# Kernel optimization log

Measured on AMD Instinct MI355X. Metric: run time of the kernel, lower is better.

The kernel has to match this reference:

```python
import jax, jax.numpy as jnp
import numpy as np

K = 4
EPS = 1e-6
NEG_INF = -1e9


def _extract_patches(x, k):
    # x: [C, H, W] -> [P, C*k*k], P = (H-k+1)*(W-k+1), p = hp*Wp + wp
    C, H, W = x.shape
    Hp, Wp = H - k + 1, W - k + 1
    cols = jnp.stack([x[:, di:di + Hp, dj:dj + Wp]
                      for di in range(k) for dj in range(k)], axis=1)  # [C, k*k, Hp, Wp]
    return cols.reshape(C * k * k, Hp * Wp).T  # [P, C*k*k]


def setup_inputs() -> dict:
    key = jax.random.key(0)
    k1, k2, k3 = jax.random.split(key, 3)
    C, H, W = 32, 80, 80
    low = jax.random.normal(k1, (1, C, H, W), dtype=jnp.float32)
    high = jax.random.normal(k2, (1, C, H, W), dtype=jnp.float32)
    mask = jax.random.randint(k3, (H + 1, W + 1), 0, 2, dtype=jnp.int32)
    return {"low_level_features": low, "hight_level_features": high, "mask": mask}


def reference(low_level_features, hight_level_features, mask):
    k = K
    low = low_level_features[0]    # [C, H, W]
    high = hight_level_features[0]
    C, H, W = low.shape
    Hp, Wp = H - k + 1, W - k + 1
    P = Hp * Wp

    low_p = _extract_patches(low, k)    # [P, D], D = C*k*k (candidate patches)
    high_p = _extract_patches(high, k)  # [P, D] (query filters)
    norms = jnp.sqrt(jnp.sum(low_p * low_p, axis=1))  # torch.norm per patch, [P]

    # all-pairs cosine-distance scores: [P_query, P_candidate]
    scores = jnp.einsum('qd,pd->qp', high_p, low_p) / (norms + EPS)[None, :]
    # candidates where mask==1 (top-left of patch) are excluded (set to inf=-1e9)
    excl = (mask[:Hp, :Wp].reshape(-1) == 1)
    scores = jnp.where(excl[None, :], NEG_INF, scores)
    best = jnp.argmax(scores, axis=1)   # [P] best match per query patch

    # a query patch at (i,j) is processed only if its 4 mask corners are nonzero
    valid = ((mask[:Hp, :Wp] != 0) & (mask[:Hp, k:k + Wp] != 0) &
             (mask[k:k + Hp, :Wp] != 0) & (mask[k:k + Hp, k:k + Wp] != 0))
    validf = valid.astype(low.dtype).reshape(-1)  # [P]

    gathered = low_p[best] * validf[:, None]            # [P, D]
    g = gathered.reshape(Hp, Wp, C, k, k)               # per-query result patches
    vmap2d = validf.reshape(Hp, Wp)

    result = jnp.zeros_like(low)
    counts = jnp.zeros((H, W), low.dtype)
    for di in range(k):
        for dj in range(k):
            result = result.at[:, di:di + Hp, dj:dj + Wp].add(
                jnp.moveaxis(g[:, :, :, di, dj], -1, 0))
            counts = counts.at[di:di + Hp, dj:dj + Wp].add(vmap2d)

    out = result / (counts + EPS)[None, :, :]
    nz = counts != 0
    out = out * nz[None, :, :] + low * (~nz)[None, :, :]
    return out[None]  # [1, C, H, W]
```

## Files before the change

### kernel.cpp

```cpp
#include <hip/hip_runtime.h>
#include <hip/hip_bf16.h>

#define CC    32
#define HH    80
#define WW    80
#define HW    6400
#define HPQ   77
#define WPQ   77
#define PP    5929
#define DD    512
#define MSTR  81
#define NTILE 93
#define QTILES 372
#define NEGINF (-1e9f)

typedef __attribute__((ext_vector_type(4))) float f32x4;
typedef __attribute__((ext_vector_type(8))) short bf16x8;
typedef __attribute__((ext_vector_type(8))) unsigned short u16x8;

__device__ __forceinline__ void split_bf16(float v, unsigned short& hi, unsigned short& lo) {
    __hip_bfloat16 h = __float2bfloat16(v);
    float hf = __bfloat162float(h);
    __hip_bfloat16 lw = __float2bfloat16(v - hf);
    hi = *reinterpret_cast<unsigned short*>(&h);
    lo = *reinterpret_cast<unsigned short*>(&lw);
}

__global__ __launch_bounds__(256) void k_main(const float* __restrict__ low,
                                              const float* __restrict__ high,
                                              const int* __restrict__ mask,
                                              float* __restrict__ invn,
                                              int* __restrict__ excl,
                                              int* __restrict__ qslot,
                                              int* __restrict__ nvalid,
                                              unsigned short* __restrict__ Bhi,
                                              unsigned short* __restrict__ Blo,
                                              unsigned short* __restrict__ Ahi,
                                              unsigned short* __restrict__ Alo) {
    const int g = blockIdx.x;
    const int tid = threadIdx.x;

    if (g >= NTILE) {
        int t = (g - NTILE) * 256 + tid;
        int l = t & 63;
        int s = (t >> 6) & 15;
        int u = t >> 10;
        int n = l & 15, quad = l >> 4;
        int p = u * 16 + n;
        int kbase = s * 32 + quad * 8;
        u16x8 vh, vl;
        if (p < PP) {
            int pi = p / WPQ, pj = p % WPQ;
            int base = (kbase >> 4) * HW + pi * WW + pj;
#pragma unroll
            for (int j = 0; j < 8; ++j) {
                int kk = kbase + j;
                int di = (kk >> 2) & 3, dj = kk & 3;
                unsigned short h, lo;
                split_bf16(low[base + di * WW + dj], h, lo);
                vh[j] = h; vl[j] = lo;
            }
        } else {
#pragma unroll
            for (int j = 0; j < 8; ++j) { vh[j] = 0; vl[j] = 0; }
        }
        int off = t * 8;
        *reinterpret_cast<u16x8*>(Bhi + off) = vh;
        *reinterpret_cast<u16x8*>(Blo + off) = vl;
        return;
    }

    __shared__ float part[4][64];
    __shared__ int s_n;
    __shared__ int s_q[64];
    __shared__ int s_slot[64];
    const int pl = tid & 63;
    const int slc = tid >> 6;
    const int p = g * 64 + pl;

    float s = 0.f;
    if (p < PP) {
        int pi = p / WPQ, pj = p % WPQ;
        int base = pi * WW + pj;
        for (int c = slc * 8; c < slc * 8 + 8; ++c) {
            int b2 = c * HW + base;
#pragma unroll
            for (int di = 0; di < 4; ++di)
#pragma unroll
                for (int dj = 0; dj < 4; ++dj) {
                    float v = low[b2 + di * WW + dj];
                    s += v * v;
                }
        }
    }
    part[slc][pl] = s;
    if (tid == 0) s_n = 0;
    __syncthreads();
    if (tid < 64 && p < PP) {
        float t4 = part[0][tid] + part[1][tid] + part[2][tid] + part[3][tid];
        invn[p] = 1.0f / (sqrtf(t4) + 1e-6f);
        int pi = p / WPQ, pj = p % WPQ;
        int m00 = mask[pi * MSTR + pj];
        int m01 = mask[pi * MSTR + pj + 4];
        int m10 = mask[(pi + 4) * MSTR + pj];
        int m11 = mask[(pi + 4) * MSTR + pj + 4];
        excl[p] = (m00 == 1) ? 1 : 0;
        int slot = -1;
        if (m00 != 0 && m01 != 0 && m10 != 0 && m11 != 0) {
            slot = atomicAdd(nvalid, 1);
            int li = atomicAdd(&s_n, 1);
            s_q[li] = p;
            s_slot[li] = slot;
        }
        qslot[p] = slot;
    }
    __syncthreads();

    const int nn = s_n;
    const int c64 = tid & 63;
    const int ss = c64 >> 2, qd = c64 & 3;
    const int kbase = ss * 32 + qd * 8;
    for (int vi = tid >> 6; vi < nn; vi += 4) {
        int q = s_q[vi], slot = s_slot[vi];
        int qi = q / WPQ, qj = q % WPQ;
        int base = (kbase >> 4) * HW + qi * WW + qj;
        u16x8 vh, vl;
#pragma unroll
        for (int j = 0; j < 8; ++j) {
            int kk = kbase + j;
            int di = (kk >> 2) & 3, dj = kk & 3;
            unsigned short h, lo;
            split_bf16(high[base + di * WW + dj], h, lo);
            vh[j] = h; vl[j] = lo;
        }
        int u = slot >> 4, m = slot & 15;
        int off = u * 8192 + ss * 512 + (qd * 16 + m) * 8;
        *reinterpret_cast<u16x8*>(Ahi + off) = vh;
        *reinterpret_cast<u16x8*>(Alo + off) = vl;
    }
}

__global__ __launch_bounds__(256) void k_score(const unsigned short* __restrict__ Ahi,
                                               const unsigned short* __restrict__ Alo,
                                               const unsigned short* __restrict__ Bhi,
                                               const unsigned short* __restrict__ Blo,
                                               const int* __restrict__ excl,
                                               const float* __restrict__ invn,
                                               const int* __restrict__ nvalid,
                                               unsigned long long* __restrict__ bestpk) {
    const int nv = *nvalid;
    const int w = threadIdx.x >> 6;
    const int l = threadIdx.x & 63;
    const int pblk = blockIdx.x;
    const int n = l & 15, quad = l >> 4;
    const int bbase = pblk * 4 * 8192 + l * 8;

    int gpv[4]; bool exv[4]; float ivv[4];
#pragma unroll
    for (int pt = 0; pt < 4; ++pt) {
        gpv[pt] = pblk * 64 + pt * 16 + n;
        if (gpv[pt] < PP) { exv[pt] = (excl[gpv[pt]] != 0); ivv[pt] = invn[gpv[pt]]; }
        else              { exv[pt] = true;                 ivv[pt] = 0.f; }
    }

    for (int qblk = blockIdx.y; qblk * 64 < nv; qblk += 12) {
        const int qtile = qblk * 4 + w;
        f32x4 acc[4];
#pragma unroll
        for (int pt = 0; pt < 4; ++pt) acc[pt] = (f32x4){0.f, 0.f, 0.f, 0.f};

        const int abase = qtile * 8192 + l * 8;
#pragma unroll 4
        for (int s = 0; s < 16; ++s) {
            bf16x8 ah = *reinterpret_cast<const bf16x8*>(Ahi + abase + s * 512);
            bf16x8 al = *reinterpret_cast<const bf16x8*>(Alo + abase + s * 512);
#pragma unroll
            for (int pt = 0; pt < 4; ++pt) {
                bf16x8 bh = *reinterpret_cast<const bf16x8*>(Bhi + bbase + pt * 8192 + s * 512);
                bf16x8 bl = *reinterpret_cast<const bf16x8*>(Blo + bbase + pt * 8192 + s * 512);
                acc[pt] = __builtin_amdgcn_mfma_f32_16x16x32_bf16(ah, bh, acc[pt], 0, 0, 0);
                acc[pt] = __builtin_amdgcn_mfma_f32_16x16x32_bf16(ah, bl, acc[pt], 0, 0, 0);
                acc[pt] = __builtin_amdgcn_mfma_f32_16x16x32_bf16(al, bh, acc[pt], 0, 0, 0);
            }
        }

        float bs[4]; int bi[4];
#pragma unroll
        for (int r = 0; r < 4; ++r) { bs[r] = -3.4e38f; bi[r] = 0x7fffffff; }
#pragma unroll
        for (int pt = 0; pt < 4; ++pt) {
            if (gpv[pt] < PP) {
#pragma unroll
                for (int r = 0; r < 4; ++r) {
                    float sv = exv[pt] ? NEGINF : acc[pt][r] * ivv[pt];
                    if (sv > bs[r]) { bs[r] = sv; bi[r] = gpv[pt]; }
                }
            }
        }
#pragma unroll
        for (int off = 1; off <= 8; off <<= 1) {
#pragma unroll
            for (int r = 0; r < 4; ++r) {
                float s2 = __shfl_xor(bs[r], off, 64);
                int   i2 = __shfl_xor(bi[r], off, 64);
                if (s2 > bs[r] || (s2 == bs[r] && i2 < bi[r])) { bs[r] = s2; bi[r] = i2; }
            }
        }
        if (n == 0) {
#pragma unroll
            for (int r = 0; r < 4; ++r) {
                if (bi[r] != 0x7fffffff) {
                    unsigned ub = __float_as_uint(bs[r]);
                    unsigned mo = (ub & 0x80000000u) ? ~ub : (ub | 0x80000000u);
                    unsigned long long pk =
                        ((unsigned long long)mo << 32) | (unsigned)(~bi[r]);
                    int slot = qtile * 16 + quad * 4 + r;
                    atomicMax(bestpk + slot, pk);
                }
            }
        }
    }
}

__global__ __launch_bounds__(256) void k_out(const float* __restrict__ low,
                                             const int* __restrict__ qslot,
                                             const unsigned long long* __restrict__ bestpk,
                                             float* __restrict__ out) {
    __shared__ int scnt[64];
    __shared__ int soff[64][17];
    const int tid = threadIdx.x;
    const int pixb = blockIdx.x * 64;
    if (tid < 64) {
        int pix = pixb + tid;
        int i = pix / WW, j = pix % WW;
        int nn = 0;
#pragma unroll
        for (int di = 0; di < 4; ++di) {
            int qi = i - di;
            if (qi < 0 || qi >= HPQ) continue;
#pragma unroll
            for (int dj = 0; dj < 4; ++dj) {
                int qj = j - dj;
                if (qj < 0 || qj >= WPQ) continue;
                int sl = qslot[qi * WPQ + qj];
                if (sl >= 0) {
                    int b = (int)(~(unsigned)bestpk[sl]);
                    soff[tid][nn++] = (b / WPQ + di) * WW + (b % WPQ + dj);
                }
            }
        }
        scnt[tid] = nn;
    }
    __syncthreads();
    const int pl = tid & 63, cg = tid >> 6;
    const int nn = scnt[pl];
    const int pix = pixb + pl;
    const float inv = 1.0f / ((float)nn + 1e-6f);
#pragma unroll
    for (int k = 0; k < 8; ++k) {
        int c = cg * 8 + k;
        int base = c * HW;
        float a;
        if (nn > 0) {
            a = 0.f;
            for (int t2 = 0; t2 < nn; ++t2) a += low[base + soff[pl][t2]];
            a *= inv;
        } else {
            a = low[base + pix];
        }
        out[base + pix] = a;
    }
}

extern "C" void kernel_launch(void* const* d_in, const int* in_sizes, int n_in,
                              void* d_out, int out_size, void* d_ws, size_t ws_size,
                              hipStream_t stream) {
    const float* low  = (const float*)d_in[0];
    const float* high = (const float*)d_in[1];
    const int*   mask = (const int*)d_in[2];
    float* out = (float*)d_out;

    char* ws = (char*)d_ws;
    int* nvalid = (int*)ws;
    unsigned long long* bestpk = (unsigned long long*)(ws + 64);
    int*   qslot = (int*)(ws + 49216);
    float* invn  = (float*)(ws + 73024);
    int*   excl  = (int*)(ws + 96832);
    unsigned short* Ahi = (unsigned short*)(ws + 120640);
    unsigned short* Alo = (unsigned short*)(ws + 6215488);
    unsigned short* Bhi = (unsigned short*)(ws + 12310336);
    unsigned short* Blo = (unsigned short*)(ws + 18405184);

    hipMemsetAsync(ws, 0, 49216, stream);
    hipLaunchKernelGGL(k_main, dim3(NTILE + QTILES * 4), dim3(256), 0, stream,
                       low, high, mask, invn, excl, qslot, nvalid, Bhi, Blo, Ahi, Alo);
    hipLaunchKernelGGL(k_score, dim3(NTILE, 12), dim3(256), 0, stream,
                       Ahi, Alo, Bhi, Blo, excl, invn, nvalid, bestpk);
    hipLaunchKernelGGL(k_out, dim3(100), dim3(256), 0, stream,
                       low, qslot, bestpk, out);
}
```

Baseline: 120.0 us.

## Fuse pack, score and output stages into one cooperative persistent kernel

Replaces the memset plus three separate launches with a single cooperative kernel of 512 persistent blocks. The phases (B packing and workspace zeroing, norms/flags/A packing, scoring, output gather) are separated by grid-wide syncs. Scoring work is distributed as flattened (pblk, qblk) pairs over the blocks. This removes launch gaps and the memset, at the cost of grid.sync overhead, idle blocks in the small phases, and a launch-bounds occupancy constraint. If the cooperative launch fails, it falls back to the old multi-kernel path.

```diff
diff --git a/kernel.cpp b/kernel.cpp
--- a/kernel.cpp
+++ b/kernel.cpp
@@ -1,5 +1,8 @@
 #include <hip/hip_runtime.h>
 #include <hip/hip_bf16.h>
+#include <hip/hip_cooperative_groups.h>
+
+namespace cg = cooperative_groups;
 
 #define CC    32
 #define HH    80
@@ -8,10 +11,10 @@
 #define HPQ   77
 #define WPQ   77
 #define PP    5929
-#define DD    512
 #define MSTR  81
 #define NTILE 93
 #define QTILES 372
+#define NBLK  512
 #define NEGINF (-1e9f)
 
 typedef __attribute__((ext_vector_type(4))) float f32x4;
@@ -24,6 +27,287 @@
     __hip_bfloat16 lw = __float2bfloat16(v - hf);
     hi = *reinterpret_cast<unsigned short*>(&h);
     lo = *reinterpret_cast<unsigned short*>(&lw);
+}
+
+
+__device__ __forceinline__ void packB_unit(const float* __restrict__ low,
+                                           unsigned short* __restrict__ Bhi,
+                                           unsigned short* __restrict__ Blo,
+                                           int unit, int tid) {
+    int t = unit * 256 + tid;
+    int l = t & 63;
+    int s = (t >> 6) & 15;
+    int u = t >> 10;
+    int n = l & 15, quad = l >> 4;
+    int p = u * 16 + n;
+    int kbase = s * 32 + quad * 8;
+    u16x8 vh, vl;
+    if (p < PP) {
+        int pi = p / WPQ, pj = p % WPQ;
+        int base = (kbase >> 4) * HW + pi * WW + pj;
+#pragma unroll
+        for (int j = 0; j < 8; ++j) {
+            int kk = kbase + j;
+            int di = (kk >> 2) & 3, dj = kk & 3;
+            unsigned short h, lo2;
+            split_bf16(low[base + di * WW + dj], h, lo2);
+            vh[j] = h; vl[j] = lo2;
+        }
+    } else {
+#pragma unroll
+        for (int j = 0; j < 8; ++j) { vh[j] = 0; vl[j] = 0; }
+    }
+    int off = t * 8;
+    *reinterpret_cast<u16x8*>(Bhi + off) = vh;
+    *reinterpret_cast<u16x8*>(Blo + off) = vl;
+}
+
+struct FlagsLds { float part[4][64]; int s_n; int s_q[64]; int s_slot[64]; };
+
+__device__ __forceinline__ void flags_block(const float* __restrict__ low,
+                                            const float* __restrict__ high,
+                                            const int* __restrict__ mask,
+                                            float* __restrict__ invn,
+                                            int* __restrict__ excl,
+                                            int* __restrict__ qslot,
+                                            int* __restrict__ nvalid,
+                                            unsigned short* __restrict__ Ahi,
+                                            unsigned short* __restrict__ Alo,
+                                            FlagsLds& L, int g, int tid) {
+    const int pl = tid & 63;
+    const int slc = tid >> 6;
+    const int p = g * 64 + pl;
+    float s = 0.f;
+    if (p < PP) {
+        int pi = p / WPQ, pj = p % WPQ;
+        int base = pi * WW + pj;
+        for (int c = slc * 8; c < slc * 8 + 8; ++c) {
+            int b2 = c * HW + base;
+#pragma unroll
+            for (int di = 0; di < 4; ++di)
+#pragma unroll
+                for (int dj = 0; dj < 4; ++dj) {
+                    float v = low[b2 + di * WW + dj];
+                    s += v * v;
+                }
+        }
+    }
+    L.part[slc][pl] = s;
+    if (tid == 0) L.s_n = 0;
+    __syncthreads();
+    if (tid < 64 && p < PP) {
+        float t4 = L.part[0][tid] + L.part[1][tid] + L.part[2][tid] + L.part[3][tid];
+        invn[p] = 1.0f / (sqrtf(t4) + 1e-6f);
+        int pi = p / WPQ, pj = p % WPQ;
+        int m00 = mask[pi * MSTR + pj];
+        int m01 = mask[pi * MSTR + pj + 4];
+        int m10 = mask[(pi + 4) * MSTR + pj];
+        int m11 = mask[(pi + 4) * MSTR + pj + 4];
+        excl[p] = (m00 == 1) ? 1 : 0;
+        int slot = -1;
+        if (m00 != 0 && m01 != 0 && m10 != 0 && m11 != 0) {
+            slot = atomicAdd(nvalid, 1);
+            int li = atomicAdd(&L.s_n, 1);
+            L.s_q[li] = p;
+            L.s_slot[li] = slot;
+        }
+        qslot[p] = slot;
+    }
+    __syncthreads();
+    const int nn = L.s_n;
+    const int c64 = tid & 63;
+    const int ss = c64 >> 2, qd = c64 & 3;
+    const int kbase = ss * 32 + qd * 8;
+    for (int vi = tid >> 6; vi < nn; vi += 4) {
+        int q = L.s_q[vi], slot = L.s_slot[vi];
+        int qi = q / WPQ, qj = q % WPQ;
+        int base = (kbase >> 4) * HW + qi * WW + qj;
+        u16x8 vh, vl;
+#pragma unroll
+        for (int j = 0; j < 8; ++j) {
+            int kk = kbase + j;
+            int di = (kk >> 2) & 3, dj = kk & 3;
+            unsigned short h, lo2;
+            split_bf16(high[base + di * WW + dj], h, lo2);
+            vh[j] = h; vl[j] = lo2;
+        }
+        int u = slot >> 4, m = slot & 15;
+        int off = u * 8192 + ss * 512 + (qd * 16 + m) * 8;
+        *reinterpret_cast<u16x8*>(Ahi + off) = vh;
+        *reinterpret_cast<u16x8*>(Alo + off) = vl;
+    }
+}
+
+__device__ __forceinline__ void score_pair(const unsigned short* __restrict__ Ahi,
+                                           const unsigned short* __restrict__ Alo,
+                                           const unsigned short* __restrict__ Bhi,
+                                           const unsigned short* __restrict__ Blo,
+                                           const int* __restrict__ excl,
+                                           const float* __restrict__ invn,
+                                           unsigned long long* __restrict__ bestpk,
+                                           int pblk, int qblk, int tid) {
+    const int w = tid >> 6;
+    const int l = tid & 63;
+    const int n = l & 15, quad = l >> 4;
+    const int qtile = qblk * 4 + w;
+    const int bbase = pblk * 4 * 8192 + l * 8;
+
+    int gpv[4]; bool exv[4]; float ivv[4];
+#pragma unroll
+    for (int pt = 0; pt < 4; ++pt) {
+        gpv[pt] = pblk * 64 + pt * 16 + n;
+        if (gpv[pt] < PP) { exv[pt] = (excl[gpv[pt]] != 0); ivv[pt] = invn[gpv[pt]]; }
+        else              { exv[pt] = true;                 ivv[pt] = 0.f; }
+    }
+
+    f32x4 acc[4];
+#pragma unroll
+    for (int pt = 0; pt < 4; ++pt) acc[pt] = (f32x4){0.f, 0.f, 0.f, 0.f};
+
+    const int abase = qtile * 8192 + l * 8;
+#pragma unroll 4
+    for (int s = 0; s < 16; ++s) {
+        bf16x8 ah = *reinterpret_cast<const bf16x8*>(Ahi + abase + s * 512);
+        bf16x8 al = *reinterpret_cast<const bf16x8*>(Alo + abase + s * 512);
+#pragma unroll
+        for (int pt = 0; pt < 4; ++pt) {
+            bf16x8 bh = *reinterpret_cast<const bf16x8*>(Bhi + bbase + pt * 8192 + s * 512);
+            bf16x8 bl = *reinterpret_cast<const bf16x8*>(Blo + bbase + pt * 8192 + s * 512);
+            acc[pt] = __builtin_amdgcn_mfma_f32_16x16x32_bf16(ah, bh, acc[pt], 0, 0, 0);
+            acc[pt] = __builtin_amdgcn_mfma_f32_16x16x32_bf16(ah, bl, acc[pt], 0, 0, 0);
+            acc[pt] = __builtin_amdgcn_mfma_f32_16x16x32_bf16(al, bh, acc[pt], 0, 0, 0);
+        }
+    }
+
+    float bs[4]; int bi[4];
+#pragma unroll
+    for (int r = 0; r < 4; ++r) { bs[r] = -3.4e38f; bi[r] = 0x7fffffff; }
+#pragma unroll
+    for (int pt = 0; pt < 4; ++pt) {
+        if (gpv[pt] < PP) {
+#pragma unroll
+            for (int r = 0; r < 4; ++r) {
+                float sv = exv[pt] ? NEGINF : acc[pt][r] * ivv[pt];
+                if (sv > bs[r]) { bs[r] = sv; bi[r] = gpv[pt]; }
+            }
+        }
+    }
+#pragma unroll
+    for (int off = 1; off <= 8; off <<= 1) {
+#pragma unroll
+        for (int r = 0; r < 4; ++r) {
+            float s2 = __shfl_xor(bs[r], off, 64);
+            int   i2 = __shfl_xor(bi[r], off, 64);
+            if (s2 > bs[r] || (s2 == bs[r] && i2 < bi[r])) { bs[r] = s2; bi[r] = i2; }
+        }
+    }
+    if (n == 0) {
+#pragma unroll
+        for (int r = 0; r < 4; ++r) {
+            if (bi[r] != 0x7fffffff) {
+                unsigned ub = __float_as_uint(bs[r]);
+                unsigned mo = (ub & 0x80000000u) ? ~ub : (ub | 0x80000000u);
+                unsigned long long pk = ((unsigned long long)mo << 32) | (unsigned)(~bi[r]);
+                int slot = qtile * 16 + quad * 4 + r;
+                atomicMax(bestpk + slot, pk);
+            }
+        }
+    }
+}
+
+struct OutLds { int scnt[64]; int soff[64][17]; };
+
+__device__ __forceinline__ void out_block(const float* __restrict__ low,
+                                          const int* __restrict__ qslot,
+                                          const unsigned long long* __restrict__ bestpk,
+                                          float* __restrict__ out,
+                                          OutLds& L, int blk, int tid) {
+    const int pixb = blk * 64;
+    if (tid < 64) {
+        int pix = pixb + tid;
+        int i = pix / WW, j = pix % WW;
+        int nn = 0;
+#pragma unroll
+        for (int di = 0; di < 4; ++di) {
+            int qi = i - di;
+            if (qi < 0 || qi >= HPQ) continue;
+#pragma unroll
+            for (int dj = 0; dj < 4; ++dj) {
+                int qj = j - dj;
+                if (qj < 0 || qj >= WPQ) continue;
+                int sl = qslot[qi * WPQ + qj];
+                if (sl >= 0) {
+                    int bb = (int)(~(unsigned)bestpk[sl]);
+                    L.soff[tid][nn++] = (bb / WPQ + di) * WW + (bb % WPQ + dj);
+                }
+            }
+        }
+        L.scnt[tid] = nn;
+    }
+    __syncthreads();
+    const int pl = tid & 63, cg2 = tid >> 6;
+    const int nn = L.scnt[pl];
+    const int pix = pixb + pl;
+    const float inv = 1.0f / ((float)nn + 1e-6f);
+#pragma unroll
+    for (int k = 0; k < 8; ++k) {
+        int c = cg2 * 8 + k;
+        int base = c * HW;
+        float a;
+        if (nn > 0) {
+            a = 0.f;
+            for (int t2 = 0; t2 < nn; ++t2) a += low[base + L.soff[pl][t2]];
+            a *= inv;
+        } else {
+            a = low[base + pix];
+        }
+        out[base + pix] = a;
+    }
+}
+
+__global__ __launch_bounds__(256, 2) void k_all(const float* __restrict__ low,
+                                                const float* __restrict__ high,
+                                                const int* __restrict__ mask,
+                                                float* __restrict__ invn,
+                                                int* __restrict__ excl,
+                                                int* __restrict__ qslot,
+                                                int* __restrict__ nvalid,
+                                                unsigned short* __restrict__ Bhi,
+                                                unsigned short* __restrict__ Blo,
+                                                unsigned short* __restrict__ Ahi,
+                                                unsigned short* __restrict__ Alo,
+                                                unsigned long long* __restrict__ bestpk,
+                                                float* __restrict__ out) {
+    cg::grid_group grid = cg::this_grid();
+    const int b = blockIdx.x;
+    const int tid = threadIdx.x;
+    __shared__ union { FlagsLds f; OutLds o; } lds;
+
+    {
+        int gt = b * 256 + tid;
+        if (gt < 6144) bestpk[gt] = 0ull;
+        if (gt == 6144) *nvalid = 0;
+        for (int unit = b; unit < QTILES * 4; unit += NBLK)
+            packB_unit(low, Bhi, Blo, unit, tid);
+    }
+    grid.sync();
+
+    if (b < NTILE)
+        flags_block(low, high, mask, invn, excl, qslot, nvalid, Ahi, Alo, lds.f, b, tid);
+    grid.sync();
+
+    {
+        const int nv = *nvalid;
+        const int nqblk = (nv + 63) >> 6;
+        const int npairs = NTILE * nqblk;
+        for (int pair = b; pair < npairs; pair += NBLK)
+            score_pair(Ahi, Alo, Bhi, Blo, excl, invn, bestpk,
+                       pair % NTILE, pair / NTILE, tid);
+    }
+    grid.sync();
+
+    if (b < 100)
+        out_block(low, qslot, bestpk, out, lds.o, b, tid);
 }
 
 __global__ __launch_bounds__(256) void k_main(const float* __restrict__ low,
@@ -38,106 +322,12 @@
                                               unsigned short* __restrict__ Ahi,
                                               unsigned short* __restrict__ Alo) {
     const int g = blockIdx.x;
-    const int tid = threadIdx.x;
-
     if (g >= NTILE) {
-        int t = (g - NTILE) * 256 + tid;
-        int l = t & 63;
-        int s = (t >> 6) & 15;
-        int u = t >> 10;
-        int n = l & 15, quad = l >> 4;
-        int p = u * 16 + n;
-        int kbase = s * 32 + quad * 8;
-        u16x8 vh, vl;
-        if (p < PP) {
-            int pi = p / WPQ, pj = p % WPQ;
-            int base = (kbase >> 4) * HW + pi * WW + pj;
-#pragma unroll
-            for (int j = 0; j < 8; ++j) {
-                int kk = kbase + j;
-                int di = (kk >> 2) & 3, dj = kk & 3;
-                unsigned short h, lo;
-                split_bf16(low[base + di * WW + dj], h, lo);
-                vh[j] = h; vl[j] = lo;
-            }
-        } else {
-#pragma unroll
-            for (int j = 0; j < 8; ++j) { vh[j] = 0; vl[j] = 0; }
-        }
-        int off = t * 8;
-        *reinterpret_cast<u16x8*>(Bhi + off) = vh;
-        *reinterpret_cast<u16x8*>(Blo + off) = vl;
+        packB_unit(low, Bhi, Blo, g - NTILE, threadIdx.x);
         return;
     }
-
-    __shared__ float part[4][64];
-    __shared__ int s_n;
-    __shared__ int s_q[64];
-    __shared__ int s_slot[64];
-    const int pl = tid & 63;
-    const int slc = tid >> 6;
-    const int p = g * 64 + pl;
-
-    float s = 0.f;
-    if (p < PP) {
-        int pi = p / WPQ, pj = p % WPQ;
-        int base = pi * WW + pj;
-        for (int c = slc * 8; c < slc * 8 + 8; ++c) {
-            int b2 = c * HW + base;
-#pragma unroll
-            for (int di = 0; di < 4; ++di)
-#pragma unroll
-                for (int dj = 0; dj < 4; ++dj) {
-                    float v = low[b2 + di * WW + dj];
-                    s += v * v;
-                }
-        }
-    }
-    part[slc][pl] = s;
-    if (tid == 0) s_n = 0;
-    __syncthreads();
-    if (tid < 64 && p < PP) {
-        float t4 = part[0][tid] + part[1][tid] + part[2][tid] + part[3][tid];
-        invn[p] = 1.0f / (sqrtf(t4) + 1e-6f);
-        int pi = p / WPQ, pj = p % WPQ;
-        int m00 = mask[pi * MSTR + pj];
-        int m01 = mask[pi * MSTR + pj + 4];
-        int m10 = mask[(pi + 4) * MSTR + pj];
-        int m11 = mask[(pi + 4) * MSTR + pj + 4];
-        excl[p] = (m00 == 1) ? 1 : 0;
-        int slot = -1;
-        if (m00 != 0 && m01 != 0 && m10 != 0 && m11 != 0) {
-            slot = atomicAdd(nvalid, 1);
-            int li = atomicAdd(&s_n, 1);
-            s_q[li] = p;
-            s_slot[li] = slot;
-        }
-        qslot[p] = slot;
-    }
-    __syncthreads();
-
-    const int nn = s_n;
-    const int c64 = tid & 63;
-    const int ss = c64 >> 2, qd = c64 & 3;
-    const int kbase = ss * 32 + qd * 8;
-    for (int vi = tid >> 6; vi < nn; vi += 4) {
-        int q = s_q[vi], slot = s_slot[vi];
-        int qi = q / WPQ, qj = q % WPQ;
-        int base = (kbase >> 4) * HW + qi * WW + qj;
-        u16x8 vh, vl;
-#pragma unroll
-        for (int j = 0; j < 8; ++j) {
-            int kk = kbase + j;
-            int di = (kk >> 2) & 3, dj = kk & 3;
-            unsigned short h, lo;
-            split_bf16(high[base + di * WW + dj], h, lo);
-            vh[j] = h; vl[j] = lo;
-        }
-        int u = slot >> 4, m = slot & 15;
-        int off = u * 8192 + ss * 512 + (qd * 16 + m) * 8;
-        *reinterpret_cast<u16x8*>(Ahi + off) = vh;
-        *reinterpret_cast<u16x8*>(Alo + off) = vl;
-    }
+    __shared__ FlagsLds L;
+    flags_block(low, high, mask, invn, excl, qslot, nvalid, Ahi, Alo, L, g, threadIdx.x);
 }
 
 __global__ __launch_bounds__(256) void k_score(const unsigned short* __restrict__ Ahi,
@@ -149,127 +339,16 @@
                                                const int* __restrict__ nvalid,
                                                unsigned long long* __restrict__ bestpk) {
     const int nv = *nvalid;
-    const int w = threadIdx.x >> 6;
-    const int l = threadIdx.x & 63;
-    const int pblk = blockIdx.x;
-    const int n = l & 15, quad = l >> 4;
-    const int bbase = pblk * 4 * 8192 + l * 8;
-
-    int gpv[4]; bool exv[4]; float ivv[4];
-#pragma unroll
-    for (int pt = 0; pt < 4; ++pt) {
-        gpv[pt] = pblk * 64 + pt * 16 + n;
-        if (gpv[pt] < PP) { exv[pt] = (excl[gpv[pt]] != 0); ivv[pt] = invn[gpv[pt]]; }
-        else              { exv[pt] = true;                 ivv[pt] = 0.f; }
-    }
-
-    for (int qblk = blockIdx.y; qblk * 64 < nv; qblk += 12) {
-        const int qtile = qblk * 4 + w;
-        f32x4 acc[4];
-#pragma unroll
-        for (int pt = 0; pt < 4; ++pt) acc[pt] = (f32x4){0.f, 0.f, 0.f, 0.f};
-
-        const int abase = qtile * 8192 + l * 8;
-#pragma unroll 4
-        for (int s = 0; s < 16; ++s) {
-            bf16x8 ah = *reinterpret_cast<const bf16x8*>(Ahi + abase + s * 512);
-            bf16x8 al = *reinterpret_cast<const bf16x8*>(Alo + abase + s * 512);
-#pragma unroll
-            for (int pt = 0; pt < 4; ++pt) {
-                bf16x8 bh = *reinterpret_cast<const bf16x8*>(Bhi + bbase + pt * 8192 + s * 512);
-                bf16x8 bl = *reinterpret_cast<const bf16x8*>(Blo + bbase + pt * 8192 + s * 512);
-                acc[pt] = __builtin_amdgcn_mfma_f32_16x16x32_bf16(ah, bh, acc[pt], 0, 0, 0);
-                acc[pt] = __builtin_amdgcn_mfma_f32_16x16x32_bf16(ah, bl, acc[pt], 0, 0, 0);
-                acc[pt] = __builtin_amdgcn_mfma_f32_16x16x32_bf16(al, bh, acc[pt], 0, 0, 0);
-            }
-        }
-
-        float bs[4]; int bi[4];
-#pragma unroll
-        for (int r = 0; r < 4; ++r) { bs[r] = -3.4e38f; bi[r] = 0x7fffffff; }
-#pragma unroll
-        for (int pt = 0; pt < 4; ++pt) {
-            if (gpv[pt] < PP) {
-#pragma unroll
-                for (int r = 0; r < 4; ++r) {
-                    float sv = exv[pt] ? NEGINF : acc[pt][r] * ivv[pt];
-                    if (sv > bs[r]) { bs[r] = sv; bi[r] = gpv[pt]; }
-                }
-            }
-        }
-#pragma unroll
-        for (int off = 1; off <= 8; off <<= 1) {
-#pragma unroll
-            for (int r = 0; r < 4; ++r) {
-                float s2 = __shfl_xor(bs[r], off, 64);
-                int   i2 = __shfl_xor(bi[r], off, 64);
-                if (s2 > bs[r] || (s2 == bs[r] && i2 < bi[r])) { bs[r] = s2; bi[r] = i2; }
-            }
-        }
-        if (n == 0) {
-#pragma unroll
-            for (int r = 0; r < 4; ++r) {
-                if (bi[r] != 0x7fffffff) {
-                    unsigned ub = __float_as_uint(bs[r]);
-                    unsigned mo = (ub & 0x80000000u) ? ~ub : (ub | 0x80000000u);
-                    unsigned long long pk =
-                        ((unsigned long long)mo << 32) | (unsigned)(~bi[r]);
-                    int slot = qtile * 16 + quad * 4 + r;
-                    atomicMax(bestpk + slot, pk);
-                }
-            }
-        }
-    }
+    for (int qblk = blockIdx.y; qblk * 64 < nv; qblk += 12)
+        score_pair(Ahi, Alo, Bhi, Blo, excl, invn, bestpk, blockIdx.x, qblk, threadIdx.x);
 }
 
 __global__ __launch_bounds__(256) void k_out(const float* __restrict__ low,
                                              const int* __restrict__ qslot,
                                              const unsigned long long* __restrict__ bestpk,
                                              float* __restrict__ out) {
-    __shared__ int scnt[64];
-    __shared__ int soff[64][17];
-    const int tid = threadIdx.x;
-    const int pixb = blockIdx.x * 64;
-    if (tid < 64) {
-        int pix = pixb + tid;
-        int i = pix / WW, j = pix % WW;
-        int nn = 0;
-#pragma unroll
-        for (int di = 0; di < 4; ++di) {
-            int qi = i - di;
-            if (qi < 0 || qi >= HPQ) continue;
-#pragma unroll
-            for (int dj = 0; dj < 4; ++dj) {
-                int qj = j - dj;
-                if (qj < 0 || qj >= WPQ) continue;
-                int sl = qslot[qi * WPQ + qj];
-                if (sl >= 0) {
-                    int b = (int)(~(unsigned)bestpk[sl]);
-                    soff[tid][nn++] = (b / WPQ + di) * WW + (b % WPQ + dj);
-                }
-            }
-        }
-        scnt[tid] = nn;
-    }
-    __syncthreads();
-    const int pl = tid & 63, cg = tid >> 6;
-    const int nn = scnt[pl];
-    const int pix = pixb + pl;
-    const float inv = 1.0f / ((float)nn + 1e-6f);
-#pragma unroll
-    for (int k = 0; k < 8; ++k) {
-        int c = cg * 8 + k;
-        int base = c * HW;
-        float a;
-        if (nn > 0) {
-            a = 0.f;
-            for (int t2 = 0; t2 < nn; ++t2) a += low[base + soff[pl][t2]];
-            a *= inv;
-        } else {
-            a = low[base + pix];
-        }
-        out[base + pix] = a;
-    }
+    __shared__ OutLds L;
+    out_block(low, qslot, bestpk, out, L, blockIdx.x, threadIdx.x);
 }
 
 extern "C" void kernel_launch(void* const* d_in, const int* in_sizes, int n_in,
@@ -291,11 +370,18 @@
     unsigned short* Bhi = (unsigned short*)(ws + 12310336);
     unsigned short* Blo = (unsigned short*)(ws + 18405184);
 
-    hipMemsetAsync(ws, 0, 49216, stream);
-    hipLaunchKernelGGL(k_main, dim3(NTILE + QTILES * 4), dim3(256), 0, stream,
-                       low, high, mask, invn, excl, qslot, nvalid, Bhi, Blo, Ahi, Alo);
-    hipLaunchKernelGGL(k_score, dim3(NTILE, 12), dim3(256), 0, stream,
-                       Ahi, Alo, Bhi, Blo, excl, invn, nvalid, bestpk);
-    hipLaunchKernelGGL(k_out, dim3(100), dim3(256), 0, stream,
-                       low, qslot, bestpk, out);
-}
+    void* args[] = {(void*)&low, (void*)&high, (void*)&mask, (void*)&invn, (void*)&excl,
+                    (void*)&qslot, (void*)&nvalid, (void*)&Bhi, (void*)&Blo,
+                    (void*)&Ahi, (void*)&Alo, (void*)&bestpk, (void*)&out};
+    hipError_t rc = hipLaunchCooperativeKernel((const void*)k_all, dim3(NBLK), dim3(256),
+                                               args, 0, stream);
+    if (rc != hipSuccess) {
+        hipMemsetAsync(ws, 0, 49216, stream);
+        hipLaunchKernelGGL(k_main, dim3(NTILE + QTILES * 4), dim3(256), 0, stream,
+                           low, high, mask, invn, excl, qslot, nvalid, Bhi, Blo, Ahi, Alo);
+        hipLaunchKernelGGL(k_score, dim3(NTILE, 12), dim3(256), 0, stream,
+                           Ahi, Alo, Bhi, Blo, excl, invn, nvalid, bestpk);
+        hipLaunchKernelGGL(k_out, dim3(100), dim3(256), 0, stream,
+                           low, qslot, bestpk, out);
+    }
+}
```

New measurement: 296.4 us. 2.47x slower.
